# Optimization experiments

Hardware: AMD Instinct MI355X
Metric: run time of the kernel (lower is better)

The kernel has to match this reference:

```python
import jax, jax.numpy as jnp
import numpy as np


def _hfreq_mask(c, scale):
    # zeros over the centered (shifted) low-frequency band, ones elsewhere
    m = np.ones((c,), dtype=np.complex64)
    m[c // 2 - c // scale: c // 2 + c // scale] = 0
    return jnp.asarray(m).reshape(1, 1, 1, c)


def setup_inputs() -> dict:
    key = jax.random.key(0)
    x = jax.random.normal(key, (32, 38, 38, 728), dtype=jnp.float32)
    return {"x": x, "scale": 4}


def reference(x, scale):
    c = x.shape[-1]
    norm = jnp.asarray(np.sqrt(c), dtype=jnp.complex64)
    X = jnp.fft.fft(x.astype(jnp.complex64), axis=-1) / norm
    X = jnp.fft.fftshift(X, axes=-1)
    X = X * _hfreq_mask(c, scale)
    X = jnp.fft.ifftshift(X, axes=-1)
    y = jnp.fft.ifft(X, axis=-1) * norm
    y = jnp.real(y).astype(jnp.float32)
    return jax.nn.relu(y)
```

## Files before the change

### kernel.cpp

```cpp
#include <hip/hip_runtime.h>
#include <hip/hip_bf16.h>

#define CC 728
#define PP 364
#define KP 384
#define KT 12
#define M_ROWS 46208
#define NWG 2166

typedef __attribute__((ext_vector_type(8))) short bf16x8;
typedef __attribute__((ext_vector_type(8))) unsigned short ushort8;
typedef __attribute__((ext_vector_type(4))) float f32x4;

__device__ __forceinline__ unsigned int f2bf(float f) {
    unsigned int u = __float_as_uint(f);
    unsigned int r = u + 0x7fffu + ((u >> 16) & 1u);
    return r >> 16;
}

__device__ __forceinline__ float bf2f(unsigned short v) {
    unsigned int u = ((unsigned int)v) << 16;
    return __uint_as_float(u);
}

__device__ __forceinline__ void gload_lds16(const void* g, void* l) {
    __builtin_amdgcn_global_load_lds(
        (const __attribute__((address_space(1))) void*)g,
        (__attribute__((address_space(3))) void*)l,
        16, 0, 0);
}

__global__ void build_bt(unsigned short* __restrict__ bt1,
                         unsigned short* __restrict__ bt2) {
    int idx = blockIdx.x * blockDim.x + threadIdx.x;
    if (idx >= 2 * KP * KP) return;
    int mat = idx / (KP * KP);
    int rem = idx % (KP * KP);
    int n = rem / KP, k = rem % KP;
    float v = 0.f;
    if (n < PP && k < PP) {
        int m = n - k - (mat == 0 ? 1 : 0);
        if (m < 0) m += PP;
        int d = 2 * m + 1;
        float t = (float)(3.14159265358979323846 * (double)d / (double)CC);
        float s = ((d >> 1) & 1) ? 1.f : -1.f;
        v = s * cosf(t) / ((float)CC * sinf(t));
    }
    (mat == 0 ? bt1 : bt2)[n * KP + k] = (unsigned short)f2bf(v);
}

__global__ void convert_deint(const float* __restrict__ x,
                              unsigned short* __restrict__ e,
                              unsigned short* __restrict__ o) {
    int id = blockIdx.x * blockDim.x + threadIdx.x;
    if (id >= M_ROWS * 48) return;
    int r  = id / 48, p8 = id % 48;
    int c0 = p8 * 16;
    ushort8 ve, vo;
#pragma unroll
    for (int j = 0; j < 8; ++j) { ve[j] = 0; vo[j] = 0; }
    if (c0 < CC) {
        const float4* src = (const float4*)(x + (size_t)r * CC + c0);
#pragma unroll
        for (int j = 0; j < 4; ++j) {
            float4 f = (c0 + 4 * j < CC) ? src[j] : make_float4(0.f, 0.f, 0.f, 0.f);
            ve[2 * j]     = (unsigned short)f2bf(f.x);
            vo[2 * j]     = (unsigned short)f2bf(f.y);
            ve[2 * j + 1] = (unsigned short)f2bf(f.z);
            vo[2 * j + 1] = (unsigned short)f2bf(f.w);
        }
    }
    *(ushort8*)(e + (size_t)r * KP + p8 * 8) = ve;
    *(ushort8*)(o + (size_t)r * KP + p8 * 8) = vo;
}

__global__ __launch_bounds__(256) void gemm_relu(
        const unsigned short* __restrict__ e,
        const unsigned short* __restrict__ o,
        const unsigned short* __restrict__ bt1,
        const unsigned short* __restrict__ bt2,
        float* __restrict__ out) {
    __shared__ unsigned short ldsE[128 * 32];
    __shared__ unsigned short ldsO[128 * 32];
    __shared__ unsigned short ldsB1[64 * 32];
    __shared__ unsigned short ldsB2[64 * 32];

    const int tid  = threadIdx.x;
    const int lane = tid & 63;
    const int wid  = tid >> 6;
    const int wr   = wid >> 1, wc = wid & 1;
    const int l15  = lane & 15, lhi = lane >> 4;

    const int NX = 8;
    int orig = blockIdx.x;
    int q = NWG / NX, r = NWG % NX;
    int xcd = orig % NX, local = orig / NX;
    int wgid = (xcd < r ? xcd * (q + 1) : r * (q + 1) + (xcd - r) * q) + local;
    const int bm  = (wgid / 6) * 128;
    const int bnp = (wgid % 6) * 64;

    f32x4 acc_e[4][2], acc_o[4][2];
#pragma unroll
    for (int i = 0; i < 4; ++i)
#pragma unroll
        for (int j = 0; j < 2; ++j)
#pragma unroll
            for (int rr = 0; rr < 4; ++rr) { acc_e[i][j][rr] = 0.f; acc_o[i][j][rr] = 0.f; }

    const int rowA = tid >> 2;
    const int cq   = tid & 3;

    for (int kt = 0; kt < KT; ++kt) {
        const int k0 = kt * 32;

#pragma unroll
        for (int i = 0; i < 2; ++i) {
            int row  = i * 64 + rowA;
            int gsrc = (cq - (row >> 1)) & 3;
            size_t so = (size_t)(bm + row) * KP + k0 + gsrc * 8;
            gload_lds16(e + so, &ldsE[(i * 256 + tid) * 8]);
            gload_lds16(o + so, &ldsO[(i * 256 + tid) * 8]);
        }
        {
            int row  = rowA;
            int gsrc = (cq - (row >> 1)) & 3;
            size_t so = (size_t)(bnp + row) * KP + k0 + gsrc * 8;
            gload_lds16(bt1 + so, &ldsB1[tid * 8]);
            gload_lds16(bt2 + so, &ldsB2[tid * 8]);
        }
        __syncthreads();

        bf16x8 aE[4], aO[4], b1[2], b2[2];
#pragma unroll
        for (int mi = 0; mi < 4; ++mi) {
            int row = wr * 64 + mi * 16 + l15;
            int c   = (lhi + (row >> 1)) & 3;
            aE[mi] = *(const bf16x8*)&ldsE[row * 32 + c * 8];
            aO[mi] = *(const bf16x8*)&ldsO[row * 32 + c * 8];
        }
#pragma unroll
        for (int nf = 0; nf < 2; ++nf) {
            int row = wc * 32 + nf * 16 + l15;
            int c   = (lhi + (row >> 1)) & 3;
            b1[nf] = *(const bf16x8*)&ldsB1[row * 32 + c * 8];
            b2[nf] = *(const bf16x8*)&ldsB2[row * 32 + c * 8];
        }
        __builtin_amdgcn_s_setprio(1);
#pragma unroll
        for (int mi = 0; mi < 4; ++mi)
#pragma unroll
            for (int nf = 0; nf < 2; ++nf) {
                acc_e[mi][nf] = __builtin_amdgcn_mfma_f32_16x16x32_bf16(
                    aO[mi], b1[nf], acc_e[mi][nf], 0, 0, 0);
                acc_o[mi][nf] = __builtin_amdgcn_mfma_f32_16x16x32_bf16(
                    aE[mi], b2[nf], acc_o[mi][nf], 0, 0, 0);
            }
        __builtin_amdgcn_s_setprio(0);
        __syncthreads();
    }

#pragma unroll
    for (int mi = 0; mi < 4; ++mi) {
#pragma unroll
        for (int nf = 0; nf < 2; ++nf) {
            int colp = bnp + wc * 32 + nf * 16 + l15;
            if (colp < PP) {
#pragma unroll
                for (int rr = 0; rr < 4; ++rr) {
                    int rowg = bm + wr * 64 + mi * 16 + lhi * 4 + rr;
                    size_t ib = (size_t)rowg * KP + colp;
                    float fe = bf2f(e[ib]);
                    float fo = bf2f(o[ib]);
                    float ye = 0.5f * fe + acc_e[mi][nf][rr];
                    float yo = 0.5f * fo + acc_o[mi][nf][rr];
                    float2 ov;
                    ov.x = ye > 0.f ? ye : 0.f;
                    ov.y = yo > 0.f ? yo : 0.f;
                    *(float2*)&out[(size_t)rowg * CC + 2 * colp] = ov;
                }
            }
        }
    }
}

extern "C" void kernel_launch(void* const* d_in, const int* in_sizes, int n_in,
                              void* d_out, int out_size, void* d_ws, size_t ws_size,
                              hipStream_t stream) {
    const float* x = (const float*)d_in[0];
    float* out = (float*)d_out;

    unsigned short* bt1 = (unsigned short*)d_ws;
    unsigned short* bt2 = bt1 + KP * KP;
    unsigned short* e   = bt2 + KP * KP;
    unsigned short* o   = e + (size_t)M_ROWS * KP;

    build_bt<<<(2 * KP * KP + 255) / 256, 256, 0, stream>>>(bt1, bt2);
    convert_deint<<<(M_ROWS * 48) / 256, 256, 0, stream>>>(x, e, o);
    gemm_relu<<<NWG, 256, 0, stream>>>(e, o, bt1, bt2, out);
}
```

Before: 116.7 us.

## Load A fragments straight to registers and double-buffer B tiles in LDS

```diff
diff --git a/kernel.cpp b/kernel.cpp
--- a/kernel.cpp
+++ b/kernel.cpp
@@ -80,10 +80,8 @@
         const unsigned short* __restrict__ bt1,
         const unsigned short* __restrict__ bt2,
         float* __restrict__ out) {
-    __shared__ unsigned short ldsE[128 * 32];
-    __shared__ unsigned short ldsO[128 * 32];
-    __shared__ unsigned short ldsB1[64 * 32];
-    __shared__ unsigned short ldsB2[64 * 32];
+    __shared__ unsigned short ldsB1[2][64 * 32];
+    __shared__ unsigned short ldsB2[2][64 * 32];
 
     const int tid  = threadIdx.x;
     const int lane = tid & 63;
@@ -107,43 +105,39 @@
 #pragma unroll
             for (int rr = 0; rr < 4; ++rr) { acc_e[i][j][rr] = 0.f; acc_o[i][j][rr] = 0.f; }
 
-    const int rowA = tid >> 2;
-    const int cq   = tid & 3;
-
-    for (int kt = 0; kt < KT; ++kt) {
-        const int k0 = kt * 32;
-
-#pragma unroll
-        for (int i = 0; i < 2; ++i) {
-            int row  = i * 64 + rowA;
-            int gsrc = (cq - (row >> 1)) & 3;
-            size_t so = (size_t)(bm + row) * KP + k0 + gsrc * 8;
-            gload_lds16(e + so, &ldsE[(i * 256 + tid) * 8]);
-            gload_lds16(o + so, &ldsO[(i * 256 + tid) * 8]);
-        }
-        {
-            int row  = rowA;
-            int gsrc = (cq - (row >> 1)) & 3;
-            size_t so = (size_t)(bnp + row) * KP + k0 + gsrc * 8;
-            gload_lds16(bt1 + so, &ldsB1[tid * 8]);
-            gload_lds16(bt2 + so, &ldsB2[tid * 8]);
-        }
-        __syncthreads();
-
-        bf16x8 aE[4], aO[4], b1[2], b2[2];
+    const int brow = tid >> 2;
+    const int bc   = tid & 3;
+    auto stageB = [&](int buf, int kt) {
+        int gsrc = (bc - (brow >> 1)) & 3;
+        size_t so = (size_t)(bnp + brow) * KP + kt * 32 + gsrc * 8;
+        gload_lds16(bt1 + so, &ldsB1[buf][tid * 8]);
+        gload_lds16(bt2 + so, &ldsB2[buf][tid * 8]);
+    };
+
+    const unsigned short* eRow[4];
+    const unsigned short* oRow[4];
+#pragma unroll
+    for (int mi = 0; mi < 4; ++mi) {
+        size_t rb = (size_t)(bm + wr * 64 + mi * 16 + l15) * KP + lhi * 8;
+        eRow[mi] = e + rb;
+        oRow[mi] = o + rb;
+    }
+    auto loadA = [&](int kt, bf16x8 (&aE)[4], bf16x8 (&aO)[4]) {
 #pragma unroll
         for (int mi = 0; mi < 4; ++mi) {
-            int row = wr * 64 + mi * 16 + l15;
-            int c   = (lhi + (row >> 1)) & 3;
-            aE[mi] = *(const bf16x8*)&ldsE[row * 32 + c * 8];
-            aO[mi] = *(const bf16x8*)&ldsO[row * 32 + c * 8];
-        }
+            aE[mi] = *(const bf16x8*)(eRow[mi] + kt * 32);
+            aO[mi] = *(const bf16x8*)(oRow[mi] + kt * 32);
+        }
+    };
+
+    auto compute = [&](int buf, const bf16x8 (&aE)[4], const bf16x8 (&aO)[4]) {
+        bf16x8 b1[2], b2[2];
 #pragma unroll
         for (int nf = 0; nf < 2; ++nf) {
             int row = wc * 32 + nf * 16 + l15;
             int c   = (lhi + (row >> 1)) & 3;
-            b1[nf] = *(const bf16x8*)&ldsB1[row * 32 + c * 8];
-            b2[nf] = *(const bf16x8*)&ldsB2[row * 32 + c * 8];
+            b1[nf] = *(const bf16x8*)&ldsB1[buf][row * 32 + c * 8];
+            b2[nf] = *(const bf16x8*)&ldsB2[buf][row * 32 + c * 8];
         }
         __builtin_amdgcn_s_setprio(1);
 #pragma unroll
@@ -156,7 +150,33 @@
                     aE[mi], b2[nf], acc_o[mi][nf], 0, 0, 0);
             }
         __builtin_amdgcn_s_setprio(0);
-        __syncthreads();
+    };
+
+    auto step = [&](int kt, int curbuf,
+                    const bf16x8 (&aEc)[4], const bf16x8 (&aOc)[4],
+                    bf16x8 (&aEn)[4], bf16x8 (&aOn)[4]) {
+        if (kt + 1 < KT) {
+            stageB(curbuf ^ 1, kt + 1);
+            loadA(kt + 1, aEn, aOn);
+            asm volatile("s_waitcnt vmcnt(18)" ::: "memory");
+        } else {
+            asm volatile("s_waitcnt vmcnt(8)" ::: "memory");
+        }
+        __builtin_amdgcn_s_barrier();
+        __builtin_amdgcn_sched_barrier(0);
+        compute(curbuf, aEc, aOc);
+        __builtin_amdgcn_s_barrier();
+        __builtin_amdgcn_sched_barrier(0);
+    };
+
+    bf16x8 aEA[4], aOA[4], aEB[4], aOB[4];
+    stageB(0, 0);
+    loadA(0, aEA, aOA);
+
+#pragma unroll
+    for (int t2 = 0; t2 < KT / 2; ++t2) {
+        step(2 * t2,     0, aEA, aOA, aEB, aOB);
+        step(2 * t2 + 1, 1, aEB, aOB, aEA, aOA);
     }
 
 #pragma unroll
```

New measurement: 172.0 us. 47.4% more time.

## Fuse fp32-to-bf16 deinterleave into GEMM by loading raw x tiles into LDS

Applied to the files above, without the earlier changes.

```diff
diff --git a/kernel.cpp b/kernel.cpp
--- a/kernel.cpp
+++ b/kernel.cpp
@@ -9,18 +9,12 @@
 #define NWG 2166
 
 typedef __attribute__((ext_vector_type(8))) short bf16x8;
-typedef __attribute__((ext_vector_type(8))) unsigned short ushort8;
 typedef __attribute__((ext_vector_type(4))) float f32x4;
 
 __device__ __forceinline__ unsigned int f2bf(float f) {
     unsigned int u = __float_as_uint(f);
     unsigned int r = u + 0x7fffu + ((u >> 16) & 1u);
     return r >> 16;
-}
-
-__device__ __forceinline__ float bf2f(unsigned short v) {
-    unsigned int u = ((unsigned int)v) << 16;
-    return __uint_as_float(u);
 }
 
 __device__ __forceinline__ void gload_lds16(const void* g, void* l) {
@@ -31,57 +25,49 @@
 }
 
 __global__ void build_bt(unsigned short* __restrict__ bt1,
-                         unsigned short* __restrict__ bt2) {
+                         unsigned short* __restrict__ bt2,
+                         unsigned short* __restrict__ btl1,
+                         unsigned short* __restrict__ btl2) {
     int idx = blockIdx.x * blockDim.x + threadIdx.x;
-    if (idx >= 2 * KP * KP) return;
-    int mat = idx / (KP * KP);
-    int rem = idx % (KP * KP);
-    int n = rem / KP, k = rem % KP;
+    if (idx >= 2 * KP * KP + 2 * KP * 32) return;
+    int n, k, mat;
+    unsigned short* dst;
+    bool valid;
+    if (idx < 2 * KP * KP) {
+        mat = idx / (KP * KP);
+        int rem = idx % (KP * KP);
+        n = rem / KP; k = rem % KP;
+        dst = (mat == 0 ? bt1 : bt2) + n * KP + k;
+        valid = (n < PP && k < PP);
+    } else {
+        int i2 = idx - 2 * KP * KP;
+        mat = i2 / (KP * 32);
+        int rem = i2 % (KP * 32);
+        n = rem / 32; k = rem % 32;
+        dst = (mat == 0 ? btl1 : btl2) + n * 32 + k;
+        valid = (n < PP && k >= 20);
+        k += 332;
+    }
     float v = 0.f;
-    if (n < PP && k < PP) {
+    if (valid) {
         int m = n - k - (mat == 0 ? 1 : 0);
-        if (m < 0) m += PP;
+        m %= PP; if (m < 0) m += PP;
         int d = 2 * m + 1;
         float t = (float)(3.14159265358979323846 * (double)d / (double)CC);
         float s = ((d >> 1) & 1) ? 1.f : -1.f;
         v = s * cosf(t) / ((float)CC * sinf(t));
     }
-    (mat == 0 ? bt1 : bt2)[n * KP + k] = (unsigned short)f2bf(v);
-}
-
-__global__ void convert_deint(const float* __restrict__ x,
-                              unsigned short* __restrict__ e,
-                              unsigned short* __restrict__ o) {
-    int id = blockIdx.x * blockDim.x + threadIdx.x;
-    if (id >= M_ROWS * 48) return;
-    int r  = id / 48, p8 = id % 48;
-    int c0 = p8 * 16;
-    ushort8 ve, vo;
-#pragma unroll
-    for (int j = 0; j < 8; ++j) { ve[j] = 0; vo[j] = 0; }
-    if (c0 < CC) {
-        const float4* src = (const float4*)(x + (size_t)r * CC + c0);
-#pragma unroll
-        for (int j = 0; j < 4; ++j) {
-            float4 f = (c0 + 4 * j < CC) ? src[j] : make_float4(0.f, 0.f, 0.f, 0.f);
-            ve[2 * j]     = (unsigned short)f2bf(f.x);
-            vo[2 * j]     = (unsigned short)f2bf(f.y);
-            ve[2 * j + 1] = (unsigned short)f2bf(f.z);
-            vo[2 * j + 1] = (unsigned short)f2bf(f.w);
-        }
-    }
-    *(ushort8*)(e + (size_t)r * KP + p8 * 8) = ve;
-    *(ushort8*)(o + (size_t)r * KP + p8 * 8) = vo;
+    *dst = (unsigned short)f2bf(v);
 }
 
 __global__ __launch_bounds__(256) void gemm_relu(
-        const unsigned short* __restrict__ e,
-        const unsigned short* __restrict__ o,
+        const float* __restrict__ x,
         const unsigned short* __restrict__ bt1,
         const unsigned short* __restrict__ bt2,
+        const unsigned short* __restrict__ btl1,
+        const unsigned short* __restrict__ btl2,
         float* __restrict__ out) {
-    __shared__ unsigned short ldsE[128 * 32];
-    __shared__ unsigned short ldsO[128 * 32];
+    __shared__ float ldsA[128 * 64];
     __shared__ unsigned short ldsB1[64 * 32];
     __shared__ unsigned short ldsB2[64 * 32];
 
@@ -107,26 +93,32 @@
 #pragma unroll
             for (int rr = 0; rr < 4; ++rr) { acc_e[i][j][rr] = 0.f; acc_o[i][j][rr] = 0.f; }
 
-    const int rowA = tid >> 2;
+    const int brow = tid >> 2;
     const int cq   = tid & 3;
 
+#pragma unroll
     for (int kt = 0; kt < KT; ++kt) {
-        const int k0 = kt * 32;
+        const int cb = (kt < 11) ? kt * 64 : 664;
 
 #pragma unroll
-        for (int i = 0; i < 2; ++i) {
-            int row  = i * 64 + rowA;
-            int gsrc = (cq - (row >> 1)) & 3;
-            size_t so = (size_t)(bm + row) * KP + k0 + gsrc * 8;
-            gload_lds16(e + so, &ldsE[(i * 256 + tid) * 8]);
-            gload_lds16(o + so, &ldsO[(i * 256 + tid) * 8]);
+        for (int i = 0; i < 8; ++i) {
+            int chunk = i * 256 + tid;
+            int row = chunk >> 4, c = chunk & 15;
+            int cs  = c ^ (row & 7);
+            gload_lds16(x + (size_t)(bm + row) * CC + cb + cs * 4,
+                        (char*)ldsA + (size_t)chunk * 16);
         }
         {
-            int row  = rowA;
-            int gsrc = (cq - (row >> 1)) & 3;
-            size_t so = (size_t)(bnp + row) * KP + k0 + gsrc * 8;
-            gload_lds16(bt1 + so, &ldsB1[tid * 8]);
-            gload_lds16(bt2 + so, &ldsB2[tid * 8]);
+            int gsrc = (cq - (brow >> 1)) & 3;
+            if (kt < 11) {
+                size_t so = (size_t)(bnp + brow) * KP + kt * 32 + gsrc * 8;
+                gload_lds16(bt1 + so, &ldsB1[tid * 8]);
+                gload_lds16(bt2 + so, &ldsB2[tid * 8]);
+            } else {
+                size_t so = (size_t)(bnp + brow) * 32 + gsrc * 8;
+                gload_lds16(btl1 + so, &ldsB1[tid * 8]);
+                gload_lds16(btl2 + so, &ldsB2[tid * 8]);
+            }
         }
         __syncthreads();
 
@@ -134,9 +126,15 @@
 #pragma unroll
         for (int mi = 0; mi < 4; ++mi) {
             int row = wr * 64 + mi * 16 + l15;
-            int c   = (lhi + (row >> 1)) & 3;
-            aE[mi] = *(const bf16x8*)&ldsE[row * 32 + c * 8];
-            aO[mi] = *(const bf16x8*)&ldsO[row * 32 + c * 8];
+            union { bf16x8 v; unsigned int u[4]; } ue, uo;
+#pragma unroll
+            for (int j = 0; j < 4; ++j) {
+                int c = (lhi * 4 + j) ^ (row & 7);
+                float4 w = *(const float4*)&ldsA[row * 64 + c * 4];
+                ue.u[j] = f2bf(w.x) | (f2bf(w.z) << 16);
+                uo.u[j] = f2bf(w.y) | (f2bf(w.w) << 16);
+            }
+            aE[mi] = ue.v; aO[mi] = uo.v;
         }
 #pragma unroll
         for (int nf = 0; nf < 2; ++nf) {
@@ -168,15 +166,14 @@
 #pragma unroll
                 for (int rr = 0; rr < 4; ++rr) {
                     int rowg = bm + wr * 64 + mi * 16 + lhi * 4 + rr;
-                    size_t ib = (size_t)rowg * KP + colp;
-                    float fe = bf2f(e[ib]);
-                    float fo = bf2f(o[ib]);
-                    float ye = 0.5f * fe + acc_e[mi][nf][rr];
-                    float yo = 0.5f * fo + acc_o[mi][nf][rr];
+                    size_t base = (size_t)rowg * CC + 2 * colp;
+                    float2 xv = *(const float2*)&x[base];
                     float2 ov;
+                    float ye = 0.5f * xv.x + acc_e[mi][nf][rr];
+                    float yo = 0.5f * xv.y + acc_o[mi][nf][rr];
                     ov.x = ye > 0.f ? ye : 0.f;
                     ov.y = yo > 0.f ? yo : 0.f;
-                    *(float2*)&out[(size_t)rowg * CC + 2 * colp] = ov;
+                    *(float2*)&out[base] = ov;
                 }
             }
         }
@@ -189,12 +186,12 @@
     const float* x = (const float*)d_in[0];
     float* out = (float*)d_out;
 
-    unsigned short* bt1 = (unsigned short*)d_ws;
-    unsigned short* bt2 = bt1 + KP * KP;
-    unsigned short* e   = bt2 + KP * KP;
-    unsigned short* o   = e + (size_t)M_ROWS * KP;
+    unsigned short* bt1  = (unsigned short*)d_ws;
+    unsigned short* bt2  = bt1 + KP * KP;
+    unsigned short* btl1 = bt2 + KP * KP;
+    unsigned short* btl2 = btl1 + KP * 32;
 
-    build_bt<<<(2 * KP * KP + 255) / 256, 256, 0, stream>>>(bt1, bt2);
-    convert_deint<<<(M_ROWS * 48) / 256, 256, 0, stream>>>(x, e, o);
-    gemm_relu<<<NWG, 256, 0, stream>>>(e, o, bt1, bt2, out);
+    int total = 2 * KP * KP + 2 * KP * 32;
+    build_bt<<<(total + 255) / 256, 256, 0, stream>>>(bt1, bt2, btl1, btl2);
+    gemm_relu<<<NWG, 256, 0, stream>>>(x, bt1, bt2, btl1, btl2, out);
 }
```

After: 130.8 us. 12.1% more time.
